# Kernel tuning notes

Hardware: AMD Instinct MI355X
Metric: run time of the kernel (lower is better)

The kernel has to match this reference:

```python
import jax, jax.numpy as jnp
import numpy as np

N, D_IN, D_OUT, H = 8192, 256, 128, 2
SLOPE = 0.2
EPS = 1e-5  # InstanceNorm2d default eps


def setup_inputs() -> dict:
    key = jax.random.key(0)
    ks = jax.random.split(key, 6)
    x = jax.random.normal(ks[0], (N, D_IN), dtype=jnp.float32)
    conn_mask = jnp.where(jax.random.uniform(ks[1], (N, N)) < 0.05, 0.0, -1e9).astype(jnp.float32)
    W = jax.random.normal(ks[2], (H, D_IN, D_OUT), dtype=jnp.float32) * 0.05
    a_src = jax.random.normal(ks[3], (H, D_OUT), dtype=jnp.float32) * 0.1
    a_tgt = jax.random.normal(ks[4], (H, D_OUT), dtype=jnp.float32) * 0.1
    W_res = jax.random.normal(ks[5], (D_OUT, D_IN), dtype=jnp.float32) * 0.05
    return {"x": x, "conn_mask": conn_mask, "W": W, "a_src": a_src, "a_tgt": a_tgt, "W_res": W_res}


def reference(x, conn_mask, W, a_src, a_tgt, W_res):
    # dropout is identity in eval mode
    proj = jnp.einsum('nd,hdf->hnf', x, W)                      # [H,N,F]
    s_src = jnp.einsum('hnf,hf->hn', proj, a_src)[:, :, None]   # [H,N,1]
    s_tgt = jnp.einsum('hnf,hf->hn', proj, a_tgt)[:, None, :]   # [H,1,N]
    scores = jax.nn.leaky_relu(s_src + s_tgt, negative_slope=SLOPE)  # [H,N,N]
    attn = jax.nn.softmax(conn_mask[None] + scores, axis=1)     # softmax over dim=1 as in torch code
    vals = jnp.einsum('hmn,hnf->hmf', attn, proj)               # bmm -> [H,N,F]
    vals = vals.mean(axis=0)                                    # head mean -> [N,F]
    # InstanceNorm2d(1, affine=False) over the whole [N,F] plane, biased variance
    mu = vals.mean()
    var = jnp.mean(jnp.square(vals - mu))
    vals_norm = (vals - mu) / jnp.sqrt(var + EPS)
    out = vals_norm + x @ W_res.T                               # residual projection (no bias)
    out = jax.nn.elu(out)
    return (out, conn_mask)
```

## Files before the change

kernel.cpp:

```cpp
#include <hip/hip_runtime.h>
#include <stdint.h>

#define NN   8192
#define DIN  256
#define FF   128
#define NF   (NN*FF)
#define SLOPE 0.2f
#define EPSI  1e-5f
#define LOG2E 1.4426950408889634f

typedef short bf16x8 __attribute__((ext_vector_type(8)));
typedef float f32x4 __attribute__((ext_vector_type(4)));
typedef float vf4 __attribute__((ext_vector_type(4)));

#define OFF_BM     0
#define OFF_RESID  (2*NF)
#define OFF_AVEC   (3*NF)
#define OFF_SS     (4*NF)
#define OFF_ST     (OFF_SS + 2*NN)
#define OFF_CSUM   (OFF_ST + 2*NN)
#define OFF_STATS  (OFF_CSUM + 2*NN)
#define OFF_NTAB   (OFF_STATS + 16)
#define OFF_VALS   (OFF_NTAB + 4*NN)
#define OFF_WT     (OFF_VALS + NF)
#define OFF_PT2    (OFF_WT + DIN*FF)
#define OFF_VPART  (OFF_PT2 + NF)

__device__ __forceinline__ float lrelu(float x) { return x >= 0.f ? x : SLOPE * x; }
__device__ __forceinline__ float exp2fast(float x) { return __builtin_amdgcn_exp2f(x); }

__device__ __forceinline__ uint32_t bfpack(float a, float b) {
  uint32_t ua = __float_as_uint(a); ua += 0x7fffu + ((ua >> 16) & 1u);
  uint32_t ub = __float_as_uint(b); ub += 0x7fffu + ((ub >> 16) & 1u);
  return (ua >> 16) | (ub & 0xffff0000u);
}
__device__ __forceinline__ uint16_t bf16c(float a) {
  uint32_t u = __float_as_uint(a); u += 0x7fffu + ((u >> 16) & 1u);
  return (uint16_t)(u >> 16);
}

__global__ __launch_bounds__(256) void k_copy(const float* __restrict__ mask, float* __restrict__ maskout,
                                              uint32_t* __restrict__ bitmask) {
  const int t = threadIdx.x;
  const int L = t & 63, wv = t >> 6;
  const int m0 = blockIdx.x * 4;
#pragma unroll
  for (int j = 0; j < 4; ++j) {
    const size_t rowoff = (size_t)(m0 + j) * NN;
    vf4 v[8];
#pragma unroll
    for (int s = 0; s < 8; ++s)
      v[s] = __builtin_nontemporal_load((const vf4*)&mask[rowoff + s * 1024 + t * 4]);
#pragma unroll
    for (int s = 0; s < 8; ++s) {
      __builtin_nontemporal_store(v[s], (vf4*)&maskout[rowoff + s * 1024 + t * 4]);
      uint32_t nib = (v[s].x > -0.5e9f ? 1u : 0u) | (v[s].y > -0.5e9f ? 2u : 0u) |
                     (v[s].z > -0.5e9f ? 4u : 0u) | (v[s].w > -0.5e9f ? 8u : 0u);
      uint32_t w = nib << (4 * (L & 7));
      w |= __shfl_xor((int)w, 1); w |= __shfl_xor((int)w, 2); w |= __shfl_xor((int)w, 4);
      if ((L & 7) == 0)
        bitmask[(m0 + j) * 256 + s * 32 + wv * 8 + (L >> 3)] = w;
    }
  }
}

__global__ __launch_bounds__(256) void k_prep(const float* __restrict__ wres, float* __restrict__ wtr,
                                              const float* __restrict__ W, const float* __restrict__ a_src,
                                              const float* __restrict__ a_tgt, float* __restrict__ avec) {
  const int b = blockIdx.x;
  if (b < 128) {
    int i = b * 256 + threadIdx.x;
    int d = i >> 7, f = i & 127;
    wtr[i] = wres[f * DIN + d];
  } else {
    int j = b - 128;
    int h = j & 1, tg = j >> 1;
    const float* a = (tg ? a_tgt : a_src) + h * FF;
    const float* Wp = W + ((size_t)h * DIN + threadIdx.x) * FF;
    float s = 0.f;
#pragma unroll 8
    for (int f = 0; f < FF; ++f) s += Wp[f] * a[f];
    avec[j * DIN + threadIdx.x] = s;
  }
}

__global__ __launch_bounds__(256) void k_ss(const float* __restrict__ x, const float* __restrict__ avec,
                                            float* __restrict__ ss, float* __restrict__ st) {
  const int lane = threadIdx.x & 63, wid = threadIdx.x >> 6;
  const int n = blockIdx.x * 4 + wid;
  float4 xv = *(const float4*)&x[n * DIN + 4 * lane];
  float4 c0 = *(const float4*)&avec[0 * DIN + 4 * lane];
  float4 c1 = *(const float4*)&avec[1 * DIN + 4 * lane];
  float4 c2 = *(const float4*)&avec[2 * DIN + 4 * lane];
  float4 c3 = *(const float4*)&avec[3 * DIN + 4 * lane];
  float v0 = xv.x * c0.x + xv.y * c0.y + xv.z * c0.z + xv.w * c0.w;
  float v1 = xv.x * c1.x + xv.y * c1.y + xv.z * c1.z + xv.w * c1.w;
  float v2 = xv.x * c2.x + xv.y * c2.y + xv.z * c2.z + xv.w * c2.w;
  float v3 = xv.x * c3.x + xv.y * c3.y + xv.z * c3.z + xv.w * c3.w;
#pragma unroll
  for (int o = 1; o < 64; o <<= 1) {
    v0 += __shfl_xor(v0, o); v1 += __shfl_xor(v1, o);
    v2 += __shfl_xor(v2, o); v3 += __shfl_xor(v3, o);
  }
  if (lane == 0) { ss[n] = v0; ss[NN + n] = v1; st[n] = v2; st[NN + n] = v3; }
}

__global__ __launch_bounds__(256) void k_gemm(const float* __restrict__ x, const float* __restrict__ Wh,
                                              const float* __restrict__ wtr, uint32_t* __restrict__ pt2,
                                              float* __restrict__ resid) {
  const int set = blockIdx.y;
  const float* __restrict__ Wsrc = (set < 2) ? (Wh + set * (DIN * FF)) : wtr;
  const int c = blockIdx.x;
  const int row0 = c * 32;
  __shared__ float xs[32 * 68];
  __shared__ uint16_t pw16[32][132];
  const int tid = threadIdx.x;
  const int ft = tid & 31, rt = tid >> 5;
  const int f0 = ft * 4, r0 = rt * 4;
  float acc[4][4];
#pragma unroll
  for (int j = 0; j < 4; ++j)
#pragma unroll
    for (int k = 0; k < 4; ++k) acc[j][k] = 0.f;

  for (int kc = 0; kc < 4; ++kc) {
    const int d0 = kc * 64;
#pragma unroll
    for (int k2 = 0; k2 < 2; ++k2) {
      int i = tid * 4 + k2 * 1024;
      int r = i >> 6, dd = i & 63;
      *(float4*)&xs[r * 68 + dd] = *(const float4*)&x[(row0 + r) * DIN + d0 + dd];
    }
    __syncthreads();
#pragma unroll
    for (int g = 0; g < 16; ++g) {
      const int dd = g * 4;
      float xr[4][4];
#pragma unroll
      for (int j = 0; j < 4; ++j) {
        float4 t = *(const float4*)&xs[(r0 + j) * 68 + dd];
        xr[j][0] = t.x; xr[j][1] = t.y; xr[j][2] = t.z; xr[j][3] = t.w;
      }
#pragma unroll
      for (int i = 0; i < 4; ++i) {
        float4 w = *(const float4*)&Wsrc[(d0 + dd + i) * FF + f0];
#pragma unroll
        for (int j = 0; j < 4; ++j) {
          float xx = xr[j][i];
          acc[j][0] += xx * w.x; acc[j][1] += xx * w.y;
          acc[j][2] += xx * w.z; acc[j][3] += xx * w.w;
        }
      }
    }
    __syncthreads();
  }

  if (set == 2) {
#pragma unroll
    for (int j = 0; j < 4; ++j)
      *(float4*)&resid[(row0 + r0 + j) * FF + f0] = make_float4(acc[j][0], acc[j][1], acc[j][2], acc[j][3]);
    return;
  }

#pragma unroll
  for (int j = 0; j < 4; ++j)
#pragma unroll
    for (int k = 0; k < 4; ++k)
      pw16[r0 + j][f0 + k] = bf16c(acc[j][k]);
  __syncthreads();

  const int half = tid >> 7, f = tid & 127;
  uint32_t wbuf[8];
#pragma unroll
  for (int i = 0; i < 8; ++i) {
    int p = half * 8 + i;
    wbuf[i] = (uint32_t)pw16[2 * p][f] | ((uint32_t)pw16[2 * p + 1][f] << 16);
  }
  uint32_t* dst = pt2 + ((c * 2 + set) * 128 + f) * 16 + half * 8;
  *(uint4*)&dst[0] = make_uint4(wbuf[0], wbuf[1], wbuf[2], wbuf[3]);
  *(uint4*)&dst[4] = make_uint4(wbuf[4], wbuf[5], wbuf[6], wbuf[7]);
}

__global__ __launch_bounds__(512) void k_csum(const uint32_t* __restrict__ bitmask, const float* __restrict__ ss,
                                              const float* __restrict__ st, float4* __restrict__ ntab) {
  __shared__ float red[2][16][32];
  const int t = threadIdx.x;
  const int ns = t & 31, slice = t >> 5;
  const int b = blockIdx.x;
  const int n = 32 * b + ns;
  const float st0 = st[n] * LOG2E, st1 = st[NN + n] * LOG2E;
  float c0 = 0.f, c1 = 0.f;
#pragma unroll 4
  for (int mi = 0; mi < 512; ++mi) {
    const int m = slice * 512 + mi;
    uint32_t bw = bitmask[m * 256 + b];
    bool e = (bw >> ns) & 1u;
    float w0 = exp2fast(lrelu(ss[m] * LOG2E + st0));
    float w1 = exp2fast(lrelu(ss[NN + m] * LOG2E + st1));
    c0 += e ? w0 : 0.f;
    c1 += e ? w1 : 0.f;
  }
  red[0][slice][ns] = c0;
  red[1][slice][ns] = c1;
  __syncthreads();
  if (t < 32) {
    float s0 = 0.f, s1 = 0.f;
#pragma unroll
    for (int k = 0; k < 16; ++k) { s0 += red[0][k][t]; s1 += red[1][k][t]; }
    int nn = 32 * b + t;
    ntab[nn] = make_float4(st[nn] * LOG2E, st[NN + nn] * LOG2E, 1.f / s0, 1.f / s1);
  }
}

__global__ __launch_bounds__(256) void k_vals(const uint32_t* __restrict__ bitmask, const uint32_t* __restrict__ pt2,
                                              const float4* __restrict__ ntab, const float* __restrict__ ss,
                                              float* __restrict__ vpart) {
  __shared__ short B2[2][8][4][16][8];
  __shared__ short A2[2][8][4][16][8];
  const int t = threadIdx.x;
  const int lane = t & 63, wid = t >> 6;
  const int m0 = blockIdx.x * 128;
  const int nc = blockIdx.y;
  const int q = lane >> 4, col = lane & 15;
  const int n2 = t & 15, mg = t >> 4;
  const int fr = t & 127, hB = t >> 7;

  float ssm0[8], ssm1[8];
#pragma unroll
  for (int p = 0; p < 8; ++p) {
    ssm0[p] = ss[m0 + mg + 16 * p] * LOG2E;
    ssm1[p] = ss[NN + m0 + mg + 16 * p] * LOG2E;
  }

  f32x4 acc[2][8];
#pragma unroll
  for (int i = 0; i < 2; ++i)
#pragma unroll
    for (int j = 0; j < 8; ++j) acc[i][j] = (f32x4){0.f, 0.f, 0.f, 0.f};

  uint32_t* B2w = (uint32_t*)&B2[0][0][0][0][0];
  uint32_t* A2w = (uint32_t*)&A2[0][0][0][0][0];

  for (int s = 0; s < 32; ++s) {
    const int n0 = nc * 1024 + s * 32;
    const uint32_t* src = pt2 + (nc * 32 + s) * 4096;
    {
      const uint4* p4 = (const uint4*)&src[t * 16];
#pragma unroll
      for (int k = 0; k < 4; ++k) {
        uint4 v = p4[k];
        *(uint4*)&B2w[(((hB * 8 + (fr >> 4)) * 4 + k) * 16 + (fr & 15)) * 4] = v;
      }
    }
    float4 na = ntab[n0 + 2 * n2];
    float4 nb = ntab[n0 + 2 * n2 + 1];
#pragma unroll
    for (int p = 0; p < 8; ++p) {
      const int ml = mg + 16 * p;
      uint32_t bw = bitmask[(size_t)(m0 + ml) * 256 + (n0 >> 5)];
      float e0a = exp2fast(lrelu(ssm0[p] + na.x)) * na.z;
      float e1a = exp2fast(lrelu(ssm1[p] + na.y)) * na.w;
      float e0b = exp2fast(lrelu(ssm0[p] + nb.x)) * nb.z;
      float e1b = exp2fast(lrelu(ssm1[p] + nb.y)) * nb.w;
      bool b0 = (bw >> (2 * n2)) & 1, b1 = (bw >> (2 * n2 + 1)) & 1;
      e0a = b0 ? e0a : 0.f; e1a = b0 ? e1a : 0.f;
      e0b = b1 ? e0b : 0.f; e1b = b1 ? e1b : 0.f;
      int base = (p * 4 + (n2 >> 2)) * 64 + mg * 4 + (n2 & 3);
      A2w[base] = bfpack(e0a, e0b);
      A2w[base + 2048] = bfpack(e1a, e1b);
    }
    __syncthreads();
    bf16x8 a00 = *(const bf16x8*)&A2[0][wid * 2][q][col][0];
    bf16x8 a01 = *(const bf16x8*)&A2[0][wid * 2 + 1][q][col][0];
    bf16x8 a10 = *(const bf16x8*)&A2[1][wid * 2][q][col][0];
    bf16x8 a11 = *(const bf16x8*)&A2[1][wid * 2 + 1][q][col][0];
#pragma unroll
    for (int ft = 0; ft < 8; ++ft) {
      bf16x8 b0 = *(const bf16x8*)&B2[0][ft][q][col][0];
      acc[0][ft] = __builtin_amdgcn_mfma_f32_16x16x32_bf16(a00, b0, acc[0][ft], 0, 0, 0);
      acc[1][ft] = __builtin_amdgcn_mfma_f32_16x16x32_bf16(a01, b0, acc[1][ft], 0, 0, 0);
      bf16x8 b1 = *(const bf16x8*)&B2[1][ft][q][col][0];
      acc[0][ft] = __builtin_amdgcn_mfma_f32_16x16x32_bf16(a10, b1, acc[0][ft], 0, 0, 0);
      acc[1][ft] = __builtin_amdgcn_mfma_f32_16x16x32_bf16(a11, b1, acc[1][ft], 0, 0, 0);
    }
    __syncthreads();
  }

  float* dst = vpart + (size_t)nc * NF;
#pragma unroll
  for (int mt2 = 0; mt2 < 2; ++mt2)
#pragma unroll
    for (int ft = 0; ft < 8; ++ft)
#pragma unroll
      for (int r = 0; r < 4; ++r) {
        int mrow = m0 + (wid * 2 + mt2) * 16 + q * 4 + r;
        dst[mrow * FF + ft * 16 + col] = 0.5f * acc[mt2][ft][r];
      }
}

__global__ __launch_bounds__(256) void k_stats(const float* __restrict__ vpart, float* __restrict__ vals,
                                               float* __restrict__ stats) {
  int i = (blockIdx.x * 256 + threadIdx.x) * 4;
  float4 a = make_float4(0.f, 0.f, 0.f, 0.f);
#pragma unroll
  for (int p = 0; p < 8; ++p) {
    float4 v = *(const float4*)&vpart[(size_t)p * NF + i];
    a.x += v.x; a.y += v.y; a.z += v.z; a.w += v.w;
  }
  *(float4*)&vals[i] = a;
  float s = a.x + a.y + a.z + a.w;
  float q = a.x * a.x + a.y * a.y + a.z * a.z + a.w * a.w;
#pragma unroll
  for (int o = 1; o < 64; o <<= 1) { s += __shfl_xor(s, o); q += __shfl_xor(q, o); }
  if ((threadIdx.x & 63) == 0) { atomicAdd(stats, s); atomicAdd(stats + 1, q); }
}

__global__ __launch_bounds__(256) void k_final(const float* __restrict__ vals, const float* __restrict__ resid,
                                               const float* __restrict__ stats, float* __restrict__ out) {
  int i = (blockIdx.x * 256 + threadIdx.x) * 4;
  float mu = stats[0] * (1.f / NF);
  float var = stats[1] * (1.f / NF) - mu * mu;
  float rs = rsqrtf(var + EPSI);
  float4 v = *(const float4*)&vals[i];
  float4 r = *(const float4*)&resid[i];
  float t0 = (v.x - mu) * rs + r.x;
  float t1 = (v.y - mu) * rs + r.y;
  float t2 = (v.z - mu) * rs + r.z;
  float t3 = (v.w - mu) * rs + r.w;
  float4 o;
  o.x = t0 > 0.f ? t0 : expm1f(t0);
  o.y = t1 > 0.f ? t1 : expm1f(t1);
  o.z = t2 > 0.f ? t2 : expm1f(t2);
  o.w = t3 > 0.f ? t3 : expm1f(t3);
  *(float4*)&out[i] = o;
}

extern "C" void kernel_launch(void* const* d_in, const int* in_sizes, int n_in,
                              void* d_out, int out_size, void* d_ws, size_t ws_size,
                              hipStream_t stream) {
  const float* x     = (const float*)d_in[0];
  const float* mask  = (const float*)d_in[1];
  const float* W     = (const float*)d_in[2];
  const float* a_src = (const float*)d_in[3];
  const float* a_tgt = (const float*)d_in[4];
  const float* wres  = (const float*)d_in[5];
  float* out = (float*)d_out;
  float* wsf = (float*)d_ws;

  uint32_t* bitmask = (uint32_t*)(wsf + OFF_BM);
  float*    resid   = wsf + OFF_RESID;
  float*    avec    = wsf + OFF_AVEC;
  float*    ss      = wsf + OFF_SS;
  float*    st      = wsf + OFF_ST;
  float*    stats   = wsf + OFF_STATS;
  float4*   ntab    = (float4*)(wsf + OFF_NTAB);
  float*    vals    = wsf + OFF_VALS;
  float*    wt      = wsf + OFF_WT;
  uint32_t* pt2     = (uint32_t*)(wsf + OFF_PT2);
  float*    vpart   = wsf + OFF_VPART;

  (void)hipMemsetAsync(stats, 0, 16 * sizeof(float), stream);

  hipLaunchKernelGGL(k_copy,  dim3(NN / 4),       dim3(256), 0, stream, mask, out + NF, bitmask);
  hipLaunchKernelGGL(k_prep,  dim3(132),          dim3(256), 0, stream, wres, wt, W, a_src, a_tgt, avec);
  hipLaunchKernelGGL(k_ss,    dim3(NN / 4),       dim3(256), 0, stream, x, avec, ss, st);
  hipLaunchKernelGGL(k_gemm,  dim3(NN / 32, 3),   dim3(256), 0, stream, x, W, wt, pt2, resid);
  hipLaunchKernelGGL(k_csum,  dim3(NN / 32),      dim3(512), 0, stream, bitmask, ss, st, ntab);
  hipLaunchKernelGGL(k_vals,  dim3(NN / 128, 8),  dim3(256), 0, stream, bitmask, pt2, ntab, ss, vpart);
  hipLaunchKernelGGL(k_stats, dim3(NF / 1024),    dim3(256), 0, stream, vpart, vals, stats);
  hipLaunchKernelGGL(k_final, dim3(NF / 1024),    dim3(256), 0, stream, vals, resid, stats, out);
}
```

Baseline: 746.3 us.

## Factor leaky-ReLU exponentials into per-node tables to remove per-edge exp

Precomputes exp2 of the source scores and their slope-scaled versions per node, and exp2 of the target scores. The branch of the leaky ReLU is then decided by a compare against a reciprocal threshold instead of computing exp per edge. Column sums and attention weights become selects and multiplies in both the sum kernel and the value kernel, and the normalisers are folded into the per-target table. This trades transcendental work per edge for extra table loads, and risks overflow or underflow when score magnitudes are large.

```diff
diff --git a/kernel.cpp b/kernel.cpp
--- a/kernel.cpp
+++ b/kernel.cpp
@@ -18,15 +18,15 @@
 #define OFF_AVEC   (3*NF)
 #define OFF_SS     (4*NF)
 #define OFF_ST     (OFF_SS + 2*NN)
-#define OFF_CSUM   (OFF_ST + 2*NN)
-#define OFF_STATS  (OFF_CSUM + 2*NN)
+#define OFF_STAB   (OFF_ST + 2*NN)
+#define OFF_STATS  (OFF_STAB + 2*NN)
 #define OFF_NTAB   (OFF_STATS + 16)
 #define OFF_VALS   (OFF_NTAB + 4*NN)
 #define OFF_WT     (OFF_VALS + NF)
 #define OFF_PT2    (OFF_WT + DIN*FF)
 #define OFF_VPART  (OFF_PT2 + NF)
-
-__device__ __forceinline__ float lrelu(float x) { return x >= 0.f ? x : SLOPE * x; }
+#define OFF_ETAB   (OFF_VPART + 8*NF)
+
 __device__ __forceinline__ float exp2fast(float x) { return __builtin_amdgcn_exp2f(x); }
 
 __device__ __forceinline__ uint32_t bfpack(float a, float b) {
@@ -85,7 +85,7 @@
 }
 
 __global__ __launch_bounds__(256) void k_ss(const float* __restrict__ x, const float* __restrict__ avec,
-                                            float* __restrict__ ss, float* __restrict__ st) {
+                                            float* __restrict__ st, float4* __restrict__ etab) {
   const int lane = threadIdx.x & 63, wid = threadIdx.x >> 6;
   const int n = blockIdx.x * 4 + wid;
   float4 xv = *(const float4*)&x[n * DIN + 4 * lane];
@@ -102,7 +102,12 @@
     v0 += __shfl_xor(v0, o); v1 += __shfl_xor(v1, o);
     v2 += __shfl_xor(v2, o); v3 += __shfl_xor(v3, o);
   }
-  if (lane == 0) { ss[n] = v0; ss[NN + n] = v1; st[n] = v2; st[NN + n] = v3; }
+  if (lane == 0) {
+    float s0 = v0 * LOG2E, s1 = v1 * LOG2E;
+    st[n] = v2 * LOG2E; st[NN + n] = v3 * LOG2E;
+    etab[n] = make_float4(exp2fast(s0), exp2fast(SLOPE * s0),
+                          exp2fast(s1), exp2fast(SLOPE * s1));
+  }
 }
 
 __global__ __launch_bounds__(256) void k_gemm(const float* __restrict__ x, const float* __restrict__ Wh,
@@ -181,40 +186,54 @@
   *(uint4*)&dst[4] = make_uint4(wbuf[4], wbuf[5], wbuf[6], wbuf[7]);
 }
 
-__global__ __launch_bounds__(512) void k_csum(const uint32_t* __restrict__ bitmask, const float* __restrict__ ss,
-                                              const float* __restrict__ st, float4* __restrict__ ntab) {
-  __shared__ float red[2][16][32];
+__global__ __launch_bounds__(512) void k_csum(const uint32_t* __restrict__ bitmask, const float4* __restrict__ etab,
+                                              const float* __restrict__ st, float4* __restrict__ ntab,
+                                              float2* __restrict__ stab) {
+  __shared__ float red[4][16][32];
   const int t = threadIdx.x;
   const int ns = t & 31, slice = t >> 5;
   const int b = blockIdx.x;
   const int n = 32 * b + ns;
-  const float st0 = st[n] * LOG2E, st1 = st[NN + n] * LOG2E;
-  float c0 = 0.f, c1 = 0.f;
+  const float st0 = st[n], st1 = st[NN + n];
+  const float F10 = exp2fast(st0), F11 = exp2fast(st1);
+  const float T0 = __builtin_amdgcn_rcpf(F10), T1 = __builtin_amdgcn_rcpf(F11);
+  float aA = 0.f, aB = 0.f, aC = 0.f, aD = 0.f;
 #pragma unroll 4
   for (int mi = 0; mi < 512; ++mi) {
     const int m = slice * 512 + mi;
     uint32_t bw = bitmask[m * 256 + b];
     bool e = (bw >> ns) & 1u;
-    float w0 = exp2fast(lrelu(ss[m] * LOG2E + st0));
-    float w1 = exp2fast(lrelu(ss[NN + m] * LOG2E + st1));
-    c0 += e ? w0 : 0.f;
-    c1 += e ? w1 : 0.f;
-  }
-  red[0][slice][ns] = c0;
-  red[1][slice][ns] = c1;
+    float4 E = etab[m];
+    bool c0 = E.x >= T0, c1 = E.z >= T1;
+    aA += (e && c0) ? E.x : 0.f;
+    aB += (e && !c0) ? E.y : 0.f;
+    aC += (e && c1) ? E.z : 0.f;
+    aD += (e && !c1) ? E.w : 0.f;
+  }
+  red[0][slice][ns] = aA; red[1][slice][ns] = aB;
+  red[2][slice][ns] = aC; red[3][slice][ns] = aD;
   __syncthreads();
   if (t < 32) {
-    float s0 = 0.f, s1 = 0.f;
-#pragma unroll
-    for (int k = 0; k < 16; ++k) { s0 += red[0][k][t]; s1 += red[1][k][t]; }
-    int nn = 32 * b + t;
-    ntab[nn] = make_float4(st[nn] * LOG2E, st[NN + nn] * LOG2E, 1.f / s0, 1.f / s1);
+    float sA = 0.f, sB = 0.f, sC = 0.f, sD = 0.f;
+#pragma unroll
+    for (int k = 0; k < 16; ++k) {
+      sA += red[0][k][t]; sB += red[1][k][t];
+      sC += red[2][k][t]; sD += red[3][k][t];
+    }
+    const int nn = 32 * b + t;
+    const float u0 = st[nn], u1 = st[NN + nn];
+    const float G1 = exp2fast(u0), G2 = exp2fast(SLOPE * u0);
+    const float H1 = exp2fast(u1), H2 = exp2fast(SLOPE * u1);
+    const float r0 = 1.f / (G1 * sA + G2 * sB);
+    const float r1 = 1.f / (H1 * sC + H2 * sD);
+    ntab[nn] = make_float4(G1 * r0, G2 * r0, H1 * r1, H2 * r1);
+    stab[nn] = make_float2(__builtin_amdgcn_rcpf(G1), __builtin_amdgcn_rcpf(H1));
   }
 }
 
 __global__ __launch_bounds__(256) void k_vals(const uint32_t* __restrict__ bitmask, const uint32_t* __restrict__ pt2,
-                                              const float4* __restrict__ ntab, const float* __restrict__ ss,
-                                              float* __restrict__ vpart) {
+                                              const float4* __restrict__ ntab, const float2* __restrict__ stab,
+                                              const float4* __restrict__ etab, float* __restrict__ vpart) {
   __shared__ short B2[2][8][4][16][8];
   __shared__ short A2[2][8][4][16][8];
   const int t = threadIdx.x;
@@ -225,12 +244,9 @@
   const int n2 = t & 15, mg = t >> 4;
   const int fr = t & 127, hB = t >> 7;
 
-  float ssm0[8], ssm1[8];
-#pragma unroll
-  for (int p = 0; p < 8; ++p) {
-    ssm0[p] = ss[m0 + mg + 16 * p] * LOG2E;
-    ssm1[p] = ss[NN + m0 + mg + 16 * p] * LOG2E;
-  }
+  float4 E[8];
+#pragma unroll
+  for (int p = 0; p < 8; ++p) E[p] = etab[m0 + mg + 16 * p];
 
   f32x4 acc[2][8];
 #pragma unroll
@@ -254,20 +270,25 @@
     }
     float4 na = ntab[n0 + 2 * n2];
     float4 nb = ntab[n0 + 2 * n2 + 1];
+    float4 sT = *(const float4*)&stab[n0 + 2 * n2];
 #pragma unroll
     for (int p = 0; p < 8; ++p) {
       const int ml = mg + 16 * p;
       uint32_t bw = bitmask[(size_t)(m0 + ml) * 256 + (n0 >> 5)];
-      float e0a = exp2fast(lrelu(ssm0[p] + na.x)) * na.z;
-      float e1a = exp2fast(lrelu(ssm1[p] + na.y)) * na.w;
-      float e0b = exp2fast(lrelu(ssm0[p] + nb.x)) * nb.z;
-      float e1b = exp2fast(lrelu(ssm1[p] + nb.y)) * nb.w;
       bool b0 = (bw >> (2 * n2)) & 1, b1 = (bw >> (2 * n2 + 1)) & 1;
-      e0a = b0 ? e0a : 0.f; e1a = b0 ? e1a : 0.f;
-      e0b = b1 ? e0b : 0.f; e1b = b1 ? e1b : 0.f;
+      bool ca = E[p].x >= sT.x;
+      float w0a = (ca ? E[p].x : E[p].y) * (ca ? na.x : na.y);
+      bool da = E[p].z >= sT.y;
+      float w1a = (da ? E[p].z : E[p].w) * (da ? na.z : na.w);
+      bool cb = E[p].x >= sT.z;
+      float w0b = (cb ? E[p].x : E[p].y) * (cb ? nb.x : nb.y);
+      bool db = E[p].z >= sT.w;
+      float w1b = (db ? E[p].z : E[p].w) * (db ? nb.z : nb.w);
+      w0a = b0 ? w0a : 0.f; w1a = b0 ? w1a : 0.f;
+      w0b = b1 ? w0b : 0.f; w1b = b1 ? w1b : 0.f;
       int base = (p * 4 + (n2 >> 2)) * 64 + mg * 4 + (n2 & 3);
-      A2w[base] = bfpack(e0a, e0b);
-      A2w[base + 2048] = bfpack(e1a, e1b);
+      A2w[base] = bfpack(w0a, w0b);
+      A2w[base + 2048] = bfpack(w1a, w1b);
     }
     __syncthreads();
     bf16x8 a00 = *(const bf16x8*)&A2[0][wid * 2][q][col][0];
@@ -350,23 +371,24 @@
   uint32_t* bitmask = (uint32_t*)(wsf + OFF_BM);
   float*    resid   = wsf + OFF_RESID;
   float*    avec    = wsf + OFF_AVEC;
-  float*    ss      = wsf + OFF_SS;
   float*    st      = wsf + OFF_ST;
+  float2*   stab    = (float2*)(wsf + OFF_STAB);
   float*    stats   = wsf + OFF_STATS;
   float4*   ntab    = (float4*)(wsf + OFF_NTAB);
   float*    vals    = wsf + OFF_VALS;
   float*    wt      = wsf + OFF_WT;
   uint32_t* pt2     = (uint32_t*)(wsf + OFF_PT2);
   float*    vpart   = wsf + OFF_VPART;
+  float4*   etab    = (float4*)(wsf + OFF_ETAB);
 
   (void)hipMemsetAsync(stats, 0, 16 * sizeof(float), stream);
 
   hipLaunchKernelGGL(k_copy,  dim3(NN / 4),       dim3(256), 0, stream, mask, out + NF, bitmask);
   hipLaunchKernelGGL(k_prep,  dim3(132),          dim3(256), 0, stream, wres, wt, W, a_src, a_tgt, avec);
-  hipLaunchKernelGGL(k_ss,    dim3(NN / 4),       dim3(256), 0, stream, x, avec, ss, st);
+  hipLaunchKernelGGL(k_ss,    dim3(NN / 4),       dim3(256), 0, stream, x, avec, st, etab);
   hipLaunchKernelGGL(k_gemm,  dim3(NN / 32, 3),   dim3(256), 0, stream, x, W, wt, pt2, resid);
-  hipLaunchKernelGGL(k_csum,  dim3(NN / 32),      dim3(512), 0, stream, bitmask, ss, st, ntab);
-  hipLaunchKernelGGL(k_vals,  dim3(NN / 128, 8),  dim3(256), 0, stream, bitmask, pt2, ntab, ss, vpart);
+  hipLaunchKernelGGL(k_csum,  dim3(NN / 32),      dim3(512), 0, stream, bitmask, etab, st, ntab, stab);
+  hipLaunchKernelGGL(k_vals,  dim3(NN / 128, 8),  dim3(256), 0, stream, bitmask, pt2, ntab, stab, etab, vpart);
   hipLaunchKernelGGL(k_stats, dim3(NF / 1024),    dim3(256), 0, stream, vpart, vals, stats);
   hipLaunchKernelGGL(k_final, dim3(NF / 1024),    dim3(256), 0, stream, vals, resid, stats, out);
 }
```

After: 732.9 us. No clear change (-1.8%).
